# Performance work log

Hardware: AMD Instinct MI355X
Metric: run time of the kernel (lower is better)

## Reference

```python
import jax, jax.numpy as jnp
import numpy as np

B = 4096      # batch
E = 128       # HP.max_entity
DENT = 256    # HP.entity_embedding_size
DK = 32       # HP.original_32 (key/query/LSTM hidden)
DAR = 1024
DH = 256      # HP.original_256 (fc1 out / LSTM input)
STEPS = E // 2  # max_selected
END = E - 1   # end-of-selection slot
NEG = -1.0e9


def setup_inputs() -> dict:
    key = jax.random.key(0)
    ks = jax.random.split(key, 12)
    s = 0.02
    return {
        "autoregressive_embedding": jax.random.normal(ks[0], (B, DAR), jnp.float32),
        "entity_embedding": jax.random.normal(ks[1], (B, E, DENT), jnp.float32),
        "select_unit_mask": jnp.ones((B, E), bool),
        "unit_num": jax.random.randint(ks[2], (B,), 1, E + 1).astype(jnp.float32),
        "conv_w": jax.random.normal(ks[3], (DK, DENT), jnp.float32) * s,
        "conv_b": jnp.zeros((DK,), jnp.float32),
        "fc1_w": jax.random.normal(ks[4], (DH, DAR), jnp.float32) * s,
        "fc1_b": jnp.zeros((DH,), jnp.float32),
        "w_ih": jax.random.normal(ks[5], (4 * DK, DH), jnp.float32) * s,
        "w_hh": jax.random.normal(ks[6], (4 * DK, DK), jnp.float32) * s,
        "b_ih": jnp.zeros((4 * DK,), jnp.float32),
        "b_hh": jnp.zeros((4 * DK,), jnp.float32),
        "proj_w": jax.random.normal(ks[7], (DAR, DK), jnp.float32) * s,
        "proj_b": jnp.zeros((DAR,), jnp.float32),
    }


def reference(autoregressive_embedding, entity_embedding, select_unit_mask, unit_num,
              conv_w, conv_b, fc1_w, fc1_b, w_ih, w_hh, b_ih, b_hh, proj_w, proj_b):
    bsz = entity_embedding.shape[0]
    # 1x1 conv over entities == per-entity linear: [B,E,DK]
    key_feat = jnp.einsum('bed,kd->bek', entity_embedding, conv_w) + conv_b
    key_avg = key_feat.sum(axis=1) / unit_num[:, None]  # [B,DK]
    rng = jax.random.key(42)
    bidx = jnp.arange(bsz)

    def step(carry, i):
        ar, h, c, mask, is_end, sel_num = carry
        x = jax.nn.relu(ar @ fc1_w.T + fc1_b)                     # [B,DH]
        gates = x @ w_ih.T + b_ih + h @ w_hh.T + b_hh             # [B,4*DK]
        gi, gf, gg, go = jnp.split(gates, 4, axis=-1)
        c = jax.nn.sigmoid(gf) * c + jax.nn.sigmoid(gi) * jnp.tanh(gg)
        h = jax.nn.sigmoid(go) * jnp.tanh(c)                      # query [B,DK]
        logits = jnp.einsum('bk,bek->be', h, key_feat)            # [B,E]
        masked = jnp.where(mask, logits, NEG)
        uid = jax.random.categorical(jax.random.fold_in(rng, i), masked)  # [B]
        mask = mask.at[bidx, uid].set(False)
        new_end = uid == END
        sel_num = jnp.where(new_end & (~is_end), i.astype(jnp.float32), sel_num)
        is_end = is_end | new_end
        out = key_feat[bidx, uid] - key_avg                       # one-hot bmm gather [B,DK]
        t = out @ proj_w.T + proj_b                               # [B,DAR]
        ar = ar + t * (~is_end)[:, None].astype(ar.dtype)
        return (ar, h, c, mask, is_end, sel_num), (masked, uid)

    init = (autoregressive_embedding,
            jnp.zeros((bsz, DK), jnp.float32),
            jnp.zeros((bsz, DK), jnp.float32),
            select_unit_mask,
            jnp.zeros((bsz,), bool),
            jnp.full((bsz,), float(STEPS), jnp.float32))
    (ar, _, _, _, _, sel_num), (logits, units) = jax.lax.scan(step, init, jnp.arange(STEPS))
    total_logits = jnp.transpose(logits, (1, 0, 2))  # [B,STEPS,E]
    units = units.T                                  # [B,STEPS]
    return total_logits, units, ar, sel_num
```

## Files before the change

kernel.cpp:

```cpp
#include <hip/hip_runtime.h>
#include <cstdint>
#include <math.h>

#define NSTEPS 64
#define NEGV   (-1.0e9f)

#define OUT_L0 0
#define OUT_U0 33554432
#define OUT_A0 33816576
#define OUT_S0 38010880

#define WS_KF  0
#define WS_KA  67108864
#define WS_M2  68157440
#define WS_VPB 68222976

#define JAX_PARTITIONABLE 1

__device__ __forceinline__ uint32_t rotl32(uint32_t x, int r){ return (x << r) | (x >> (32 - r)); }

__device__ __forceinline__ void threefry2x32(uint32_t k0, uint32_t k1,
                                             uint32_t x0, uint32_t x1,
                                             uint32_t &o0, uint32_t &o1){
  const uint32_t ks2 = k0 ^ k1 ^ 0x1BD11BDAu;
  x0 += k0; x1 += k1;
#define TFR(r) { x0 += x1; x1 = rotl32(x1, (r)); x1 ^= x0; }
  TFR(13) TFR(15) TFR(26) TFR(6)
  x0 += k1;  x1 += ks2 + 1u;
  TFR(17) TFR(29) TFR(16) TFR(24)
  x0 += ks2; x1 += k0 + 2u;
  TFR(13) TFR(15) TFR(26) TFR(6)
  x0 += k0;  x1 += k1 + 3u;
  TFR(17) TFR(29) TFR(16) TFR(24)
  x0 += k1;  x1 += ks2 + 4u;
  TFR(13) TFR(15) TFR(26) TFR(6)
  x0 += ks2; x1 += k0 + 5u;
#undef TFR
  o0 = x0; o1 = x1;
}

__device__ __forceinline__ float gumbel_bits_f32(uint32_t bits){
  float f = __uint_as_float(0x3F800000u | (bits >> 9)) - 1.0f;
  float u = (f == 0.0f) ? 1.17549435e-38f : f;
  return -__logf(-__logf(u));
}

__device__ __forceinline__ uint32_t jax_bits(uint32_t k0, uint32_t k1, uint32_t j){
#if JAX_PARTITIONABLE
  uint32_t o0, o1;
  threefry2x32(k0, k1, 0u, j, o0, o1);
  return o0 ^ o1;
#else
  const uint32_t HALF = 262144u;
  uint32_t o0, o1;
  if (j < HALF){ threefry2x32(k0, k1, j, j + HALF, o0, o1); return o0; }
  else         { threefry2x32(k0, k1, j - HALF, j, o0, o1); return o1; }
#endif
}

__launch_bounds__(256, 4)
__global__ void k_keyfeat(const float* __restrict__ ee, const float* __restrict__ convw,
                          const float* __restrict__ convb, float* __restrict__ kf){
  __shared__ float wlds[32 * 260];
  __shared__ float elds[8 * 256];
  const int t = threadIdx.x;
  for (int j = 0; j < 32; ++j){
    int idx = t + 256 * j;
    int k = idx >> 8, d = idx & 255;
    wlds[k * 260 + d] = convw[idx];
  }
  __syncthreads();
  const int r8 = t >> 5, k = t & 31;
  const float bk = convb[k];
  const long rowbase = (long)blockIdx.x * 256;
  for (int it = 0; it < 32; ++it){
    long r0 = rowbase + it * 8;
    #pragma unroll
    for (int j = 0; j < 2; ++j){
      int f = t + 256 * j;
      int rr = f >> 6, d4 = (f & 63) << 2;
      *reinterpret_cast<float4*>(&elds[rr * 256 + d4]) =
        *reinterpret_cast<const float4*>(&ee[(r0 + rr) * 256 + d4]);
    }
    __syncthreads();
    float c0 = 0.f, c1 = 0.f, c2 = 0.f, c3 = 0.f;
    #pragma unroll 8
    for (int d4 = 0; d4 < 256; d4 += 4){
      float4 e4 = *reinterpret_cast<const float4*>(&elds[r8 * 256 + d4]);
      float4 w4 = *reinterpret_cast<const float4*>(&wlds[k * 260 + d4]);
      c0 = fmaf(e4.x, w4.x, c0); c1 = fmaf(e4.y, w4.y, c1);
      c2 = fmaf(e4.z, w4.z, c2); c3 = fmaf(e4.w, w4.w, c3);
    }
    double s = ((double)c0 + (double)c1) + ((double)c2 + (double)c3) + (double)bk;
    kf[(r0 + r8) * 32 + k] = (float)s;
    __syncthreads();
  }
}

__global__ void k_keyavg(const float* __restrict__ kf, const float* __restrict__ unum,
                         double* __restrict__ ka){
  const int t = threadIdx.x;
  const int b = blockIdx.x * 8 + (t >> 5), k = t & 31;
  const float* p = kf + (long)b * 4096 + k;
  double s = 0.0;
  #pragma unroll 8
  for (int e = 0; e < 128; ++e) s += (double)p[e * 32];
  ka[b * 32 + k] = s / (double)unum[b];
}

__global__ void k_m2(const float* __restrict__ fc1w, const float* __restrict__ projw,
                     const float* __restrict__ projb, double* __restrict__ m2,
                     double* __restrict__ vpb){
  const int t = threadIdx.x;
  if (blockIdx.x < 32){
    const int o = blockIdx.x * 8 + (t >> 5), k = t & 31;
    double s = 0.0;
    for (int d = 0; d < 1024; ++d)
      s = fma((double)fc1w[o * 1024 + d], (double)projw[d * 32 + k], s);
    m2[o * 32 + k] = s;
  } else {
    const int o = t;
    double s = 0.0;
    for (int d = 0; d < 1024; ++d)
      s = fma((double)fc1w[o * 1024 + d], (double)projb[d], s);
    vpb[o] = s;
  }
}

#define SM_KF   0
#define SM_X    131072
#define SM_GL   140288
#define SM_H    148480
#define SM_OV   150528
#define SM_KA   152576
#define SM_KEYS 154624
#define SM_GT   155136
#define SM_CNT  155200
#define SM_HF   155264
#define SM_OVF  156288
#define SM_SIZE 157312

__launch_bounds__(512, 2)
__global__ void k_scan(const float* __restrict__ ar0, const void* __restrict__ selmask,
                       const float* __restrict__ fc1w, const float* __restrict__ fc1b,
                       const float* __restrict__ wih, const float* __restrict__ whh,
                       const float* __restrict__ bih, const float* __restrict__ bhh,
                       const float* __restrict__ projw, const float* __restrict__ projb,
                       const float* __restrict__ kfg, const double* __restrict__ kag,
                       const double* __restrict__ m2g, const double* __restrict__ vpbg,
                       float* __restrict__ outp){
  extern __shared__ char smem[];
  float4* kf4 = (float4*)(smem + SM_KF);
  float*  xk  = (float*) (smem + SM_X);
  double* gl  = (double*)(smem + SM_GL);
  double* hld = (double*)(smem + SM_H);
  double* ovd = (double*)(smem + SM_OV);
  double* kav = (double*)(smem + SM_KA);
  uint2*  keys= (uint2*) (smem + SM_KEYS);
  double* gted= (double*)(smem + SM_GT);
  double* cntd= (double*)(smem + SM_CNT);
  float*  hf  = (float*) (smem + SM_HF);
  float*  ovf = (float*) (smem + SM_OVF);

  const int t  = threadIdx.x;
  const int w  = t >> 6;
  const int ln = t & 63;
  const int o  = t & 255;
  const int rh = t >> 8;
  const int g  = t >> 2;
  const int sh = t & 3;
  const long blkrow = (long)blockIdx.x * 8;

  if (t < NSTEPS){
    uint32_t o0, o1; threefry2x32(0u, 42u, 0u, (uint32_t)t, o0, o1);
    keys[t] = make_uint2(o0, o1);
  }
  float* arst = (float*)(smem + SM_KF);
  #pragma unroll
  for (int j = 0; j < 4; ++j){
    int f = t + 512 * j;
    int r = f >> 8, d4 = (f & 255) << 2;
    *reinterpret_cast<float4*>(&arst[r * 1024 + d4]) =
      *reinterpret_cast<const float4*>(&ar0[(blkrow + r) * 1024 + d4]);
  }
  if (t < 256){
    int r = t >> 5, k = t & 31;
    kav[r * 32 + k] = kag[(blkrow + r) * 32 + k];
  }
  __syncthreads();

  double z[4];
  {
    float a[4][4] = {{0.f,0.f,0.f,0.f},{0.f,0.f,0.f,0.f},{0.f,0.f,0.f,0.f},{0.f,0.f,0.f,0.f}};
    const float* wr = fc1w + (long)o * 1024;
    #pragma unroll 4
    for (int d4 = 0; d4 < 1024; d4 += 4){
      float4 w4 = *reinterpret_cast<const float4*>(&wr[d4]);
      #pragma unroll
      for (int q = 0; q < 4; ++q){
        float4 av = *reinterpret_cast<const float4*>(&arst[(rh * 4 + q) * 1024 + d4]);
        a[q][0] = fmaf(w4.x, av.x, a[q][0]); a[q][1] = fmaf(w4.y, av.y, a[q][1]);
        a[q][2] = fmaf(w4.z, av.z, a[q][2]); a[q][3] = fmaf(w4.w, av.w, a[q][3]);
      }
    }
    const double bb = (double)fc1b[o];
    #pragma unroll
    for (int q = 0; q < 4; ++q)
      z[q] = ((double)a[q][0] + (double)a[q][1]) + ((double)a[q][2] + (double)a[q][3]) + bb;
  }
  __syncthreads();

  #pragma unroll
  for (int j = 0; j < 16; ++j){
    int f = t + 512 * j;
    int r = f >> 10, rem = f & 1023;
    int e = rem >> 3, sl = rem & 7;
    float4 v = *reinterpret_cast<const float4*>(&kfg[((blkrow + r) * 128 + e) * 32 + sl * 4]);
    kf4[(r * 128 + e) * 8 + (sl ^ (e & 7))] = v;
  }

  float m2rf[32];
  #pragma unroll
  for (int k = 0; k < 32; ++k) m2rf[k] = (float)m2g[o * 32 + k];
  const double vpbr = vpbg[o];
  float4 w4r[16];
  #pragma unroll
  for (int j = 0; j < 16; ++j)
    w4r[j] = *reinterpret_cast<const float4*>(&wih[g * 256 + sh * 64 + j * 4]);
  float whr[8];
  #pragma unroll
  for (int jk = 0; jk < 8; ++jk) whr[jk] = whh[g * 32 + sh * 8 + jk];
  const double bsum = (double)bih[g] + (double)bhh[g];

  uint64_t m0, m1;
  {
    const uint32_t w0 = *(const uint32_t*)selmask;
    if (w0 == 0x01010101u){
      const uint8_t* m8 = (const uint8_t*)selmask;
      m0 = __ballot(m8[(blkrow + w) * 128 + ln] != 0);
      m1 = __ballot(m8[(blkrow + w) * 128 + 64 + ln] != 0);
    } else {
      const uint32_t* m32 = (const uint32_t*)selmask;
      m0 = __ballot(m32[(blkrow + w) * 128 + ln] != 0);
      m1 = __ballot(m32[(blkrow + w) * 128 + 64 + ln] != 0);
    }
  }
  bool  isend = false;
  float selnum = (float)NSTEPS;
  double cnt_reg = 0.0;
  float  c_regf = 0.f;
  double sacc_reg = 0.0;
  if (ln < 32){ hld[w * 32 + ln] = 0.0; hf[w * 32 + ln] = 0.f; }
  __syncthreads();

  #pragma unroll 1
  for (int i = 0; i < NSTEPS; ++i){
    #pragma unroll
    for (int q = 0; q < 4; ++q){
      double zv = z[q];
      float xv = zv > 0.0 ? (float)zv : 0.0f;
      xk[(rh * 4 + q) * 288 + (o >> 5) * 36 + (o & 31)] = xv;
    }
    __syncthreads();

    {
      float acc[8] = {0.f,0.f,0.f,0.f,0.f,0.f,0.f,0.f};
      #pragma unroll
      for (int i4 = 0; i4 < 64; i4 += 4){
        const int d = sh * 64 + i4;
        const int xi = (d >> 5) * 36 + (d & 31);
        const float4 w4 = w4r[i4 >> 2];
        #pragma unroll
        for (int r = 0; r < 8; ++r){
          float4 xv = *reinterpret_cast<const float4*>(&xk[r * 288 + xi]);
          acc[r] = fmaf(w4.x, xv.x, fmaf(w4.y, xv.y, fmaf(w4.z, xv.z, fmaf(w4.w, xv.w, acc[r]))));
        }
      }
      #pragma unroll
      for (int r = 0; r < 8; ++r){
        float hacc = 0.f;
        #pragma unroll
        for (int q2 = 0; q2 < 2; ++q2){
          float4 hv = *reinterpret_cast<const float4*>(&hf[r * 32 + sh * 8 + q2 * 4]);
          const float* wp = &whr[q2 * 4];
          hacc = fmaf(wp[0], hv.x, fmaf(wp[1], hv.y,
                 fmaf(wp[2], hv.z, fmaf(wp[3], hv.w, hacc))));
        }
        acc[r] += hacc;
      }
      #pragma unroll
      for (int r = 0; r < 8; ++r){
        acc[r] += __shfl_xor(acc[r], 1);
        acc[r] += __shfl_xor(acc[r], 2);
      }
      if (sh == 0){
        #pragma unroll
        for (int r = 0; r < 8; ++r) gl[r * 128 + g] = (double)acc[r] + bsum;
      }
    }
    __syncthreads();

    if (ln < 32){
      const int k = ln;
      float gi = (float)gl[w * 128 + k],      gf = (float)gl[w * 128 + 32 + k];
      float gc = (float)gl[w * 128 + 64 + k], go = (float)gl[w * 128 + 96 + k];
      float ig = 1.f / (1.f + __expf(-gi));
      float fg = 1.f / (1.f + __expf(-gf));
      float og = 1.f / (1.f + __expf(-go));
      float tg = 2.f / (1.f + __expf(-2.f * gc)) - 1.f;
      c_regf = fg * c_regf + ig * tg;
      float tc = 2.f / (1.f + __expf(-2.f * c_regf)) - 1.f;
      float hv = og * tc;
      hld[w * 32 + k] = (double)hv;
      hf[w * 32 + k] = hv;
    }
    __syncthreads();

    double lg[2];
    const size_t lbase = ((size_t)(blkrow + w) * NSTEPS + i) * 128;
    #pragma unroll
    for (int j = 0; j < 2; ++j){
      const int e = ln + 64 * j;
      const int sw = e & 7;
      const int base = (w * 128 + e) * 8;
      double acc = 0.0;
      #pragma unroll
      for (int l = 0; l < 8; ++l){
        float4 v = kf4[base + (l ^ sw)];
        const double* hp = &hld[w * 32 + l * 4];
        acc = fma((double)v.x, hp[0], acc);
        acc = fma((double)v.y, hp[1], acc);
        acc = fma((double)v.z, hp[2], acc);
        acc = fma((double)v.w, hp[3], acc);
      }
      lg[j] = acc;
      bool bit = (j == 0) ? ((m0 >> e) & 1ull) : ((m1 >> (e - 64)) & 1ull);
      outp[OUT_L0 + lbase + e] = bit ? (float)acc : NEGV;
    }

    float bs = -3.0e38f; int bi = 1 << 20;
    const uint2 kk = keys[i];
    #pragma unroll
    for (int j = 0; j < 2; ++j){
      const int e = ln + 64 * j;
      bool bit = (j == 0) ? ((m0 >> e) & 1ull) : ((m1 >> (e - 64)) & 1ull);
      if (bit){
        uint32_t bits = jax_bits(kk.x, kk.y, (uint32_t)((blkrow + w) * 128 + e));
        float sv = (float)lg[j] + gumbel_bits_f32(bits);
        if (sv > bs || (sv == bs && e < bi)){ bs = sv; bi = e; }
      }
    }
    #pragma unroll
    for (int m = 1; m < 64; m <<= 1){
      float os = __shfl_xor(bs, m);
      int   oi = __shfl_xor(bi, m);
      if (os > bs || (os == bs && oi < bi)){ bs = os; bi = oi; }
    }
    const int uid = bi;

    {
      const bool new_end = (uid == 127);
      if (ln == 0 && new_end && !isend) selnum = (float)i;
      isend = isend || new_end;
      const double gate = isend ? 0.0 : 1.0;
      if (uid < 64) m0 &= ~(1ull << uid); else m1 &= ~(1ull << (uid - 64));
      if (ln == 0){
        gted[w] = gate;
        cnt_reg += gate;
        outp[OUT_U0 + (size_t)(blkrow + w) * NSTEPS + i] = (float)uid;
      }
      if (ln < 32){
        const int k = ln;
        float4 v = kf4[(w * 128 + uid) * 8 + ((k >> 2) ^ (uid & 7))];
        const int s3 = k & 3;
        float kv = (s3 == 0) ? v.x : (s3 == 1) ? v.y : (s3 == 2) ? v.z : v.w;
        double ov = (double)kv - kav[w * 32 + k];
        ovf[w * 32 + k] = (float)ov;
        sacc_reg += gate * ov;
      }
    }
    __syncthreads();

    #pragma unroll
    for (int q = 0; q < 4; ++q){
      const int r = rh * 4 + q;
      if (gted[r] != 0.0){
        float zf = 0.f;
        #pragma unroll
        for (int j8 = 0; j8 < 8; ++j8){
          float4 ov4 = *reinterpret_cast<const float4*>(&ovf[r * 32 + j8 * 4]);
          const float* mp = &m2rf[j8 * 4];
          zf = fmaf(mp[0], ov4.x, fmaf(mp[1], ov4.y,
               fmaf(mp[2], ov4.z, fmaf(mp[3], ov4.w, zf))));
        }
        z[q] += (double)zf + vpbr;
      }
    }
    __syncthreads();
  }

  if (ln < 32) ovd[w * 32 + ln] = sacc_reg;
  if (ln == 0){
    cntd[w] = cnt_reg;
    outp[OUT_S0 + (blkrow + w)] = selnum;
  }
  __syncthreads();

  #pragma unroll
  for (int jj = 0; jj < 2; ++jj){
    const int dd = t * 2 + jj;
    float4 pw4[8];
    #pragma unroll
    for (int q = 0; q < 8; ++q)
      pw4[q] = *reinterpret_cast<const float4*>(&projw[dd * 32 + q * 4]);
    const double pb = (double)projb[dd];
    #pragma unroll
    for (int r = 0; r < 8; ++r){
      const double* sp = &ovd[r * 32];
      double acc = 0.0;
      #pragma unroll
      for (int q = 0; q < 8; ++q){
        acc = fma((double)pw4[q].x, sp[q * 4 + 0], acc);
        acc = fma((double)pw4[q].y, sp[q * 4 + 1], acc);
        acc = fma((double)pw4[q].z, sp[q * 4 + 2], acc);
        acc = fma((double)pw4[q].w, sp[q * 4 + 3], acc);
      }
      double arv = (double)ar0[(blkrow + r) * 1024 + dd] + acc + pb * cntd[r];
      outp[OUT_A0 + (size_t)(blkrow + r) * 1024 + dd] = (float)arv;
    }
  }
}

extern "C" void kernel_launch(void* const* d_in, const int* in_sizes, int n_in,
                              void* d_out, int out_size, void* d_ws, size_t ws_size,
                              hipStream_t stream){
  const float*   ar0   = (const float*)d_in[0];
  const float*   ee    = (const float*)d_in[1];
  const void*    msk   = (const void*)d_in[2];
  const float*   unum  = (const float*)d_in[3];
  const float*   convw = (const float*)d_in[4];
  const float*   convb = (const float*)d_in[5];
  const float*   fc1w  = (const float*)d_in[6];
  const float*   fc1b  = (const float*)d_in[7];
  const float*   wih   = (const float*)d_in[8];
  const float*   whh   = (const float*)d_in[9];
  const float*   bih   = (const float*)d_in[10];
  const float*   bhh   = (const float*)d_in[11];
  const float*   projw = (const float*)d_in[12];
  const float*   projb = (const float*)d_in[13];
  float* out = (float*)d_out;
  char*  ws  = (char*)d_ws;

  float*  kf  = (float*) (ws + WS_KF);
  double* ka  = (double*)(ws + WS_KA);
  double* m2  = (double*)(ws + WS_M2);
  double* vpb = (double*)(ws + WS_VPB);

  k_keyfeat<<<2048, 256, 0, stream>>>(ee, convw, convb, kf);
  k_keyavg <<<512, 256, 0, stream>>>(kf, unum, ka);
  k_m2     <<<33, 256, 0, stream>>>(fc1w, projw, projb, m2, vpb);

  (void)hipFuncSetAttribute((const void*)k_scan,
                            hipFuncAttributeMaxDynamicSharedMemorySize, SM_SIZE);
  k_scan<<<512, 512, SM_SIZE, stream>>>(ar0, msk, fc1w, fc1b, wih, whh, bih, bhh,
                                        projw, projb, kf, ka, m2, vpb, out);
}
```

Baseline: 1.468 ms.

## Keep conv weights in registers for key features and parallelise fc1·proj precompute

The key-feature kernel now keeps each thread's slice of the conv weight in registers, processes 16 entity rows per tile and reduces partial dot products with warp shuffles, dropping the shared-memory weight copy and the double-precision final sum. The fused fc1·proj weight precompute is split over 256 blocks with 8 chunks per output row and a shared-memory reduction, where before 32 blocks each ran a serial 1024-long loop. This targets the prologue kernels ahead of the main scan. It trades higher register pressure for the weights and a slightly different float summation order in key_feat, which could shift sampled indices.

Measured after the change: 1.709 ms. 16.4% more time.

```diff
diff --git a/kernel.cpp b/kernel.cpp
--- a/kernel.cpp
+++ b/kernel.cpp
@@ -58,42 +58,45 @@
 #endif
 }
 
-__launch_bounds__(256, 4)
+__launch_bounds__(256, 2)
 __global__ void k_keyfeat(const float* __restrict__ ee, const float* __restrict__ convw,
                           const float* __restrict__ convb, float* __restrict__ kf){
-  __shared__ float wlds[32 * 260];
-  __shared__ float elds[8 * 256];
+  __shared__ float elds[16 * 256];
   const int t = threadIdx.x;
-  for (int j = 0; j < 32; ++j){
-    int idx = t + 256 * j;
-    int k = idx >> 8, d = idx & 255;
-    wlds[k * 260 + d] = convw[idx];
-  }
-  __syncthreads();
-  const int r8 = t >> 5, k = t & 31;
+  const int k = t >> 3;
+  const int oct = t & 7;
+  float4 wv[8];
+  #pragma unroll
+  for (int j = 0; j < 8; ++j)
+    wv[j] = *reinterpret_cast<const float4*>(&convw[k * 256 + oct * 32 + j * 4]);
   const float bk = convb[k];
   const long rowbase = (long)blockIdx.x * 256;
-  for (int it = 0; it < 32; ++it){
-    long r0 = rowbase + it * 8;
-    #pragma unroll
-    for (int j = 0; j < 2; ++j){
+  for (int tile = 0; tile < 16; ++tile){
+    const long r0 = rowbase + tile * 16;
+    __syncthreads();
+    #pragma unroll
+    for (int j = 0; j < 4; ++j){
       int f = t + 256 * j;
       int rr = f >> 6, d4 = (f & 63) << 2;
       *reinterpret_cast<float4*>(&elds[rr * 256 + d4]) =
         *reinterpret_cast<const float4*>(&ee[(r0 + rr) * 256 + d4]);
     }
     __syncthreads();
-    float c0 = 0.f, c1 = 0.f, c2 = 0.f, c3 = 0.f;
-    #pragma unroll 8
-    for (int d4 = 0; d4 < 256; d4 += 4){
-      float4 e4 = *reinterpret_cast<const float4*>(&elds[r8 * 256 + d4]);
-      float4 w4 = *reinterpret_cast<const float4*>(&wlds[k * 260 + d4]);
-      c0 = fmaf(e4.x, w4.x, c0); c1 = fmaf(e4.y, w4.y, c1);
-      c2 = fmaf(e4.z, w4.z, c2); c3 = fmaf(e4.w, w4.w, c3);
-    }
-    double s = ((double)c0 + (double)c1) + ((double)c2 + (double)c3) + (double)bk;
-    kf[(r0 + r8) * 32 + k] = (float)s;
-    __syncthreads();
+    #pragma unroll 4
+    for (int r = 0; r < 16; ++r){
+      float c0 = 0.f, c1 = 0.f, c2 = 0.f, c3 = 0.f;
+      #pragma unroll
+      for (int j = 0; j < 8; ++j){
+        float4 e4 = *reinterpret_cast<const float4*>(&elds[r * 256 + oct * 32 + j * 4]);
+        c0 = fmaf(e4.x, wv[j].x, c0); c1 = fmaf(e4.y, wv[j].y, c1);
+        c2 = fmaf(e4.z, wv[j].z, c2); c3 = fmaf(e4.w, wv[j].w, c3);
+      }
+      float s = (c0 + c1) + (c2 + c3);
+      s += __shfl_xor(s, 1);
+      s += __shfl_xor(s, 2);
+      s += __shfl_xor(s, 4);
+      if (oct == 0) kf[(r0 + r) * 32 + k] = s + bk;
+    }
   }
 }
 
@@ -112,12 +115,23 @@
                      const float* __restrict__ projb, double* __restrict__ m2,
                      double* __restrict__ vpb){
   const int t = threadIdx.x;
-  if (blockIdx.x < 32){
-    const int o = blockIdx.x * 8 + (t >> 5), k = t & 31;
+  if (blockIdx.x < 256){
+    const int o = blockIdx.x, k = t & 31, ch = t >> 5;
+    __shared__ double red[8][32];
     double s = 0.0;
-    for (int d = 0; d < 1024; ++d)
-      s = fma((double)fc1w[o * 1024 + d], (double)projw[d * 32 + k], s);
-    m2[o * 32 + k] = s;
+    const float* fw = &fc1w[o * 1024 + ch * 128];
+    const float* pw = &projw[(ch * 128) * 32 + k];
+    #pragma unroll 4
+    for (int d = 0; d < 128; ++d)
+      s = fma((double)fw[d], (double)pw[d * 32], s);
+    red[ch][k] = s;
+    __syncthreads();
+    if (ch == 0){
+      double tot = 0.0;
+      #pragma unroll
+      for (int c = 0; c < 8; ++c) tot += red[c][k];
+      m2[o * 32 + k] = tot;
+    }
   } else {
     const int o = t;
     double s = 0.0;
@@ -458,7 +472,7 @@
 
   k_keyfeat<<<2048, 256, 0, stream>>>(ee, convw, convb, kf);
   k_keyavg <<<512, 256, 0, stream>>>(kf, unum, ka);
-  k_m2     <<<33, 256, 0, stream>>>(fc1w, projw, projb, m2, vpb);
+  k_m2     <<<257, 256, 0, stream>>>(fc1w, projw, projb, m2, vpb);
 
   (void)hipFuncSetAttribute((const void*)k_scan,
                             hipFuncAttributeMaxDynamicSharedMemorySize, SM_SIZE);
```
